# Performance work log

Hardware: AMD Instinct MI355X
Metric: run time of the kernel (lower is better)

The kernel has to match this reference:

```python
import jax, jax.numpy as jnp
import numpy as np

V, E, H, K, B, T = 50000, 128, 256, 9, 128, 512
HD = H // 2  # hidden per direction


def setup_inputs() -> dict:
    key = jax.random.key(0)
    ks = jax.random.split(key, 16)
    s = 0.1
    inp = {
        "x": jax.random.randint(ks[0], (B, T), 0, V),
        "emb": jax.random.normal(ks[1], (V, E), jnp.float32) * 0.02,
        "w_ih_f": jax.random.normal(ks[2], (4 * HD, E), jnp.float32) * s,
        "w_hh_f": jax.random.normal(ks[3], (4 * HD, HD), jnp.float32) * s,
        "b_ih_f": jax.random.normal(ks[4], (4 * HD,), jnp.float32) * s,
        "b_hh_f": jax.random.normal(ks[5], (4 * HD,), jnp.float32) * s,
        "w_ih_b": jax.random.normal(ks[6], (4 * HD, E), jnp.float32) * s,
        "w_hh_b": jax.random.normal(ks[7], (4 * HD, HD), jnp.float32) * s,
        "b_ih_b": jax.random.normal(ks[8], (4 * HD,), jnp.float32) * s,
        "b_hh_b": jax.random.normal(ks[9], (4 * HD,), jnp.float32) * s,
        "W_tag": jax.random.normal(ks[10], (K, H), jnp.float32) * s,
        "b_tag": jax.random.normal(ks[11], (K,), jnp.float32) * s,
        "start_trans": jax.random.normal(ks[12], (K,), jnp.float32) * s,
        "end_trans": jax.random.normal(ks[13], (K,), jnp.float32) * s,
        "trans": jax.random.normal(ks[14], (K, K), jnp.float32) * s,
    }
    return inp


def _lstm_dir(xs, w_ih, w_hh, b_ih, b_hh, reverse):
    # xs: [T, B, E]; PyTorch gate order: i, f, g, o
    Bsz = xs.shape[1]
    hd = w_hh.shape[1]
    b = b_ih + b_hh

    def step(carry, x_t):
        h, c = carry
        gates = x_t @ w_ih.T + h @ w_hh.T + b  # [B, 4*hd]
        i, f, g, o = jnp.split(gates, 4, axis=-1)
        i = jax.nn.sigmoid(i)
        f = jax.nn.sigmoid(f)
        g = jnp.tanh(g)
        o = jax.nn.sigmoid(o)
        c = f * c + i * g
        h = o * jnp.tanh(c)
        return (h, c), h

    init = (jnp.zeros((Bsz, hd), xs.dtype), jnp.zeros((Bsz, hd), xs.dtype))
    _, hs = jax.lax.scan(step, init, xs, reverse=reverse)
    return hs  # [T, B, hd], time-ordered


def _viterbi(emissions, start_trans, end_trans, trans):
    # emissions: [T, B, K]; returns best tag path [B, T] (torchcrf decode, no mask)
    score0 = start_trans[None, :] + emissions[0]  # [B, K]

    def step(score, emis_t):
        # score[b, i] + trans[i, j] -> best over i
        cand = score[:, :, None] + trans[None, :, :]  # [B, K, K]
        bp = jnp.argmax(cand, axis=1)                 # [B, K] best prev tag
        best = jnp.max(cand, axis=1)
        return best + emis_t, bp

    final_score, bps = jax.lax.scan(step, score0, emissions[1:])  # bps: [T-1, B, K]
    final_score = final_score + end_trans[None, :]
    last_tag = jnp.argmax(final_score, axis=-1)  # [B]

    def back(tag, bp):
        prev = jnp.take_along_axis(bp, tag[:, None], axis=1)[:, 0]
        return prev, prev

    _, path = jax.lax.scan(back, last_tag, bps, reverse=True)  # [T-1, B]
    tags = jnp.concatenate([path, last_tag[None, :]], axis=0)  # [T, B]
    return tags.T.astype(jnp.int32)  # [B, T]


def reference(x, emb, w_ih_f, w_hh_f, b_ih_f, b_hh_f,
              w_ih_b, w_hh_b, b_ih_b, b_hh_b,
              W_tag, b_tag, start_trans, end_trans, trans):
    xt = x.T                        # [T, B]
    e = emb[xt]                     # [T, B, E] embedding gather
    h_f = _lstm_dir(e, w_ih_f, w_hh_f, b_ih_f, b_hh_f, reverse=False)
    h_b = _lstm_dir(e, w_ih_b, w_hh_b, b_ih_b, b_hh_b, reverse=True)
    h = jnp.concatenate([h_f, h_b], axis=-1)  # [T, B, H]
    # dropout is identity at inference
    emissions = h @ W_tag.T + b_tag           # [T, B, K]
    return _viterbi(emissions, start_trans, end_trans, trans)
```

## Files before the change

kernel.cpp:

```cpp
#include <hip/hip_runtime.h>
#include <math.h>

#define TT 512
#define BB 128
#define KK 9

__device__ __forceinline__ float fast_sigmoid(float x) {
    const float LOG2E = 1.4426950408889634f;
    float e = __builtin_amdgcn_exp2f(-x * LOG2E);
    return __builtin_amdgcn_rcpf(1.0f + e);
}
__device__ __forceinline__ float fast_tanh(float x) {
    const float LOG2E = 1.4426950408889634f;
    float a = fabsf(x);
    float e = __builtin_amdgcn_exp2f(-2.0f * a * LOG2E);
    float t = (1.0f - e) * __builtin_amdgcn_rcpf(1.0f + e);
    return copysignf(t, x);
}

__global__ __launch_bounds__(256, 3) void input_gemm(
    const int* __restrict__ x, const float* __restrict__ emb,
    const float* __restrict__ w_ih_f, const float* __restrict__ w_ih_b,
    const float* __restrict__ b_ih_f, const float* __restrict__ b_hh_f,
    const float* __restrict__ b_ih_b, const float* __restrict__ b_hh_b,
    float* __restrict__ buf_f, float* __restrict__ buf_b,
    int t0f, int t0b)
{
    const int dir = blockIdx.z;
    const int s   = blockIdx.x;
    const int n0  = blockIdx.y * 128;
    const int t   = (dir ? t0b : t0f) + s;
    const float* w  = dir ? w_ih_b : w_ih_f;
    const float* bi = dir ? b_ih_b : b_ih_f;
    const float* bh = dir ? b_hh_b : b_hh_f;
    float* dst = dir ? buf_b : buf_f;

    __shared__ __align__(16) float As[32][132];
    __shared__ __align__(16) float Bs[32][132];

    const int tid  = threadIdx.x;
    const int lrow = tid >> 3;
    const int k4   = (tid & 7) * 4;

    int tokr[4];
    #pragma unroll
    for (int p = 0; p < 4; p++) tokr[p] = x[(p * 32 + lrow) * TT + t];

    const int tx = tid & 15;
    const int ty = tid >> 4;

    float acc[8][8];
    #pragma unroll
    for (int i = 0; i < 8; i++)
        #pragma unroll
        for (int j = 0; j < 8; j++) acc[i][j] = 0.0f;

    float4 aS[4], bS[4];
    #pragma unroll
    for (int p = 0; p < 4; p++) {
        aS[p] = *(const float4*)(emb + (size_t)tokr[p] * 128 + k4);
        bS[p] = *(const float4*)(w + (size_t)(n0 + p * 32 + lrow) * 128 + k4);
    }

    for (int kc = 0; kc < 128; kc += 32) {
        __syncthreads();
        #pragma unroll
        for (int p = 0; p < 4; p++) {
            const int row = p * 32 + lrow;
            As[k4 + 0][row] = aS[p].x; As[k4 + 1][row] = aS[p].y;
            As[k4 + 2][row] = aS[p].z; As[k4 + 3][row] = aS[p].w;
            Bs[k4 + 0][row] = bS[p].x; Bs[k4 + 1][row] = bS[p].y;
            Bs[k4 + 2][row] = bS[p].z; Bs[k4 + 3][row] = bS[p].w;
        }
        __syncthreads();
        if (kc + 32 < 128) {
            #pragma unroll
            for (int p = 0; p < 4; p++) {
                aS[p] = *(const float4*)(emb + (size_t)tokr[p] * 128 + kc + 32 + k4);
                bS[p] = *(const float4*)(w + (size_t)(n0 + p * 32 + lrow) * 128 + kc + 32 + k4);
            }
        }
        #pragma unroll 8
        for (int k = 0; k < 32; k++) {
            float4 af0 = *(const float4*)&As[k][ty * 8];
            float4 af1 = *(const float4*)&As[k][ty * 8 + 4];
            float4 bf0 = *(const float4*)&Bs[k][tx * 4];
            float4 bf1 = *(const float4*)&Bs[k][64 + tx * 4];
            float a_[8] = {af0.x, af0.y, af0.z, af0.w, af1.x, af1.y, af1.z, af1.w};
            float b_[8] = {bf0.x, bf0.y, bf0.z, bf0.w, bf1.x, bf1.y, bf1.z, bf1.w};
            #pragma unroll
            for (int i = 0; i < 8; i++)
                #pragma unroll
                for (int j = 0; j < 8; j++)
                    acc[i][j] += a_[i] * b_[j];
        }
    }

    const int nb0 = n0 + tx * 4;
    const int nb1 = n0 + 64 + tx * 4;
    float bias[8];
    #pragma unroll
    for (int j = 0; j < 4; j++) {
        bias[j]     = bi[nb0 + j] + bh[nb0 + j];
        bias[4 + j] = bi[nb1 + j] + bh[nb1 + j];
    }
    #pragma unroll
    for (int i = 0; i < 8; i++) {
        int brow = ty * 8 + i;
        float* o = dst + ((size_t)s * 128 + brow) * 512;
        float4 v0, v1;
        v0.x = acc[i][0] + bias[0]; v0.y = acc[i][1] + bias[1];
        v0.z = acc[i][2] + bias[2]; v0.w = acc[i][3] + bias[3];
        v1.x = acc[i][4] + bias[4]; v1.y = acc[i][5] + bias[5];
        v1.z = acc[i][6] + bias[6]; v1.w = acc[i][7] + bias[7];
        *(float4*)(o + nb0) = v0;
        *(float4*)(o + nb1) = v1;
    }
}

__global__ __launch_bounds__(512, 2) void lstm_fused(
    const float* __restrict__ buf_f, const float* __restrict__ buf_b,
    const float* __restrict__ w_hh_f, const float* __restrict__ w_hh_b,
    float* __restrict__ h_all,
    float* __restrict__ h_state, float* __restrict__ c_state,
    const float* __restrict__ W_tag, const float* __restrict__ b_tag,
    const float* __restrict__ start_trans, const float* __restrict__ end_trans,
    const float* __restrict__ trans,
    float* __restrict__ emB, unsigned* __restrict__ flags,
    int* __restrict__ out,
    int t0f, int t0b, int C, int init, int tail)
{
    const int dir = blockIdx.x >> 7;
    const int b   = blockIdx.x & 127;
    const int j   = threadIdx.x;
    const int w_  = j >> 6;
    const int l   = j & 63;
    const int m   = l >> 2;
    const int q   = l & 3;
    const int k   = w_ * 16 + m;
    const int r   = q * 128 + k;

    unsigned snap = 0u;
    if (tail && dir == 0 && j == 0)
        snap = __hip_atomic_load(&flags[b], __ATOMIC_RELAXED, __HIP_MEMORY_SCOPE_AGENT);

    const float* whh = dir ? w_hh_b : w_hh_f;
    float wR[128];
    #pragma unroll
    for (int qq = 0; qq < 32; qq++) {
        float4 v = *(const float4*)(whh + (size_t)r * 128 + qq * 4);
        wR[4*qq+0] = v.x; wR[4*qq+1] = v.y; wR[4*qq+2] = v.z; wR[4*qq+3] = v.w;
    }

    __shared__ __align__(16) float h_lds[2][128];
    __shared__ __align__(16) float wt_s[KK * 132];
    __shared__ __align__(16) float em_s[TT * KK];
    __shared__ __align__(16) float h_tile[64 * 132];
    __shared__ unsigned char bp[TT][KK];

    float c;
    if (init) {
        c = 0.0f;
        if (q == 0) h_lds[0][k] = 0.0f;
    } else {
        c = c_state[((size_t)dir * 128 + b) * 128 + k];
        if (q == 0) h_lds[0][k] = h_state[((size_t)dir * 128 + b) * 128 + k];
    }
    __syncthreads();

    const float* buf = dir ? buf_b : buf_f;
    const int t0     = dir ? t0b : t0f;
    const int  tl0   = dir ? (C - 1) : 0;
    const long lstep = dir ? -(long)(128 * 512) : (long)(128 * 512);

    const float* xp = buf + ((size_t)tl0 * 128 + b) * 512 + r;
    float xw = *xp;
    float h_reg = 0.0f;

    float* hdst = h_all + (size_t)(dir * BB + b) * TT * 128;

    for (int s = 0; s < C; s++) {
        const int t = t0 + (dir ? (C - 1 - s) : s);
        const int p = s & 1;
        const float* hprev = h_lds[p];

        float a0 = 0.f, a1 = 0.f, a2 = 0.f, a3 = 0.f;
        #pragma unroll
        for (int qq = 0; qq < 32; qq++) {
            float4 h4 = *(const float4*)&hprev[4 * qq];
            a0 += wR[4*qq+0] * h4.x;
            a1 += wR[4*qq+1] * h4.y;
            a2 += wR[4*qq+2] * h4.z;
            a3 += wR[4*qq+3] * h4.w;
        }
        float pre = xw + ((a0 + a1) + (a2 + a3));

        float act = (q == 2) ? fast_tanh(pre) : fast_sigmoid(pre);

        float f_ = __shfl_xor(act, 1);
        float g_ = __shfl_xor(act, 2);
        float o_ = __shfl_xor(act, 3);

        c = f_ * c + act * g_;
        h_reg = o_ * fast_tanh(c);
        if (q == 0) h_lds[p ^ 1][k] = h_reg;

        __syncthreads();

        if (s + 1 < C) { xp += lstep; xw = *xp; }
        if (q == 0)
            hdst[(size_t)t * 128 + k] = h_reg;
    }

    if (q == 0) {
        h_state[((size_t)dir * 128 + b) * 128 + k] = h_reg;
        c_state[((size_t)dir * 128 + b) * 128 + k] = c;
    }

    if (!tail) return;

    for (int f = j; f < KK * 128; f += 512)
        wt_s[(f >> 7) * 132 + (f & 127)] = W_tag[(f >> 7) * 256 + dir * 128 + (f & 127)];

    float* emdst = emB + (size_t)b * TT * KK;

    for (int tile = 0; tile < TT / 64; tile++) {
        const int tb = tile * 64;
        __syncthreads();
        #pragma unroll
        for (int it = 0; it < 4; it++) {
            const int f4 = it * 512 + j;
            const int tr = f4 >> 5;
            const int c4 = (f4 & 31) * 4;
            float4 v = *(const float4*)(hdst + (size_t)(tb + tr) * 128 + c4);
            *(float4*)&h_tile[tr * 132 + c4] = v;
        }
        __syncthreads();
        for (int task = j; task < 64 * KK; task += 512) {
            const int tl = task / 9;
            const int kk = task - tl * 9;
            const float* hp = &h_tile[tl * 132];
            const float* wp = &wt_s[kk * 132];
            float acc = 0.0f;
            #pragma unroll
            for (int i4 = 0; i4 < 32; i4++) {
                float4 h4 = *(const float4*)(hp + i4 * 4);
                float4 w4 = *(const float4*)(wp + i4 * 4);
                acc += h4.x * w4.x + h4.y * w4.y + h4.z * w4.z + h4.w * w4.w;
            }
            if (dir == 1) emdst[(size_t)tb * KK + task] = acc;
            else          em_s[tb * KK + task] = acc;
        }
    }
    __syncthreads();

    if (dir == 1) {
        if (j == 0) {
            __threadfence();
            __hip_atomic_fetch_add(&flags[b], 1u, __ATOMIC_RELEASE,
                                   __HIP_MEMORY_SCOPE_AGENT);
        }
        return;
    }

    if (j == 0) {
        while (__hip_atomic_load(&flags[b], __ATOMIC_ACQUIRE,
                                 __HIP_MEMORY_SCOPE_AGENT) == snap)
            __builtin_amdgcn_s_sleep(1);
    }
    __syncthreads();
    for (int f = j; f < TT * KK; f += 512)
        em_s[f] += emdst[f] + b_tag[f % KK];
    __syncthreads();

    if (j < 64) {
        const int lane = j;

        float trans_col[KK];
        float score = -1e30f;
        if (lane < KK) {
            #pragma unroll
            for (int i = 0; i < KK; i++) trans_col[i] = trans[i * KK + lane];
            score = start_trans[lane] + em_s[lane];
        }

        float em_cur = (lane < KK) ? em_s[KK + lane] : 0.0f;
        for (int t = 1; t < TT; t++) {
            float em_next = (t + 1 < TT && lane < KK) ? em_s[(t + 1) * KK + lane] : 0.0f;

            float my = (lane < KK) ? score : -1e30f;
            float cand[KK];
            #pragma unroll
            for (int i = 0; i < KK; i++) cand[i] = __shfl(my, i) + trans_col[i];

            float v01, v23, v45, v67, v03, v47, v07, vb_;
            int   i01, i23, i45, i67, i03, i47, i07, ib_;
            {
                bool gt;
                gt = cand[1] > cand[0]; v01 = gt ? cand[1] : cand[0]; i01 = gt ? 1 : 0;
                gt = cand[3] > cand[2]; v23 = gt ? cand[3] : cand[2]; i23 = gt ? 3 : 2;
                gt = cand[5] > cand[4]; v45 = gt ? cand[5] : cand[4]; i45 = gt ? 5 : 4;
                gt = cand[7] > cand[6]; v67 = gt ? cand[7] : cand[6]; i67 = gt ? 7 : 6;
                gt = v23 > v01; v03 = gt ? v23 : v01; i03 = gt ? i23 : i01;
                gt = v67 > v45; v47 = gt ? v67 : v45; i47 = gt ? i67 : i45;
                gt = v47 > v03; v07 = gt ? v47 : v03; i07 = gt ? i47 : i03;
                gt = cand[8] > v07; vb_ = gt ? cand[8] : v07; ib_ = gt ? 8 : i07;
            }

            if (lane < KK) {
                bp[t][lane] = (unsigned char)ib_;
                score = vb_ + em_cur;
            }
            em_cur = em_next;
        }

        float fin = (lane < KK) ? (score + end_trans[lane]) : -1e30f;
        float farr[KK];
        #pragma unroll
        for (int jx = 0; jx < KK; jx++) farr[jx] = __shfl(fin, jx);
        float v01, v23, v45, v67, v03, v47, v07, vb_;
        int   i01, i23, i45, i67, i03, i47, i07, bj;
        {
            bool gt;
            gt = farr[1] > farr[0]; v01 = gt ? farr[1] : farr[0]; i01 = gt ? 1 : 0;
            gt = farr[3] > farr[2]; v23 = gt ? farr[3] : farr[2]; i23 = gt ? 3 : 2;
            gt = farr[5] > farr[4]; v45 = gt ? farr[5] : farr[4]; i45 = gt ? 5 : 4;
            gt = farr[7] > farr[6]; v67 = gt ? farr[7] : farr[6]; i67 = gt ? 7 : 6;
            gt = v23 > v01; v03 = gt ? v23 : v01; i03 = gt ? i23 : i01;
            gt = v67 > v45; v47 = gt ? v67 : v45; i47 = gt ? i67 : i45;
            gt = v47 > v03; v07 = gt ? v47 : v03; i07 = gt ? i47 : i03;
            gt = farr[8] > v07; vb_ = gt ? farr[8] : v07; bj = gt ? 8 : i07;
        }

        if (lane == 0) {
            int tag = bj;
            out[b * TT + (TT - 1)] = tag;
            for (int t = TT - 1; t >= 1; t--) {
                tag = bp[t][tag];
                out[b * TT + t - 1] = tag;
            }
        }
    }
}

extern "C" void kernel_launch(void* const* d_in, const int* in_sizes, int n_in,
                              void* d_out, int out_size, void* d_ws, size_t ws_size,
                              hipStream_t stream)
{
    const int*   x       = (const int*)  d_in[0];
    const float* emb     = (const float*)d_in[1];
    const float* w_ih_f  = (const float*)d_in[2];
    const float* w_hh_f  = (const float*)d_in[3];
    const float* b_ih_f  = (const float*)d_in[4];
    const float* b_hh_f  = (const float*)d_in[5];
    const float* w_ih_b  = (const float*)d_in[6];
    const float* w_hh_b  = (const float*)d_in[7];
    const float* b_ih_b  = (const float*)d_in[8];
    const float* b_hh_b  = (const float*)d_in[9];
    const float* W_tag   = (const float*)d_in[10];
    const float* b_tag   = (const float*)d_in[11];
    const float* start_t = (const float*)d_in[12];
    const float* end_t   = (const float*)d_in[13];
    const float* trans   = (const float*)d_in[14];
    int* out = (int*)d_out;

    const size_t em_elems    = (size_t)BB * TT * KK;
    const size_t state_elems = (size_t)2 * 128 * 128;
    const size_t hall_elems  = (size_t)2 * BB * TT * 128;

    int C = 32;
    const int cands[5] = {512, 256, 128, 64, 32};
    for (int ci = 0; ci < 5; ci++) {
        size_t need = ((size_t)2 * cands[ci] * BB * 512
                       + em_elems + 2 * state_elems + hall_elems) * sizeof(float)
                      + 1024;
        if (ws_size >= need) { C = cands[ci]; break; }
    }

    float* buf_f   = (float*)d_ws;
    float* buf_b   = buf_f + (size_t)C * BB * 512;
    float* emB     = buf_b + (size_t)C * BB * 512;
    float* h_state = emB + em_elems;
    float* c_state = h_state + state_elems;
    float* h_all   = c_state + state_elems;
    unsigned* flags = (unsigned*)(h_all + hall_elems);

    const int rounds = TT / C;
    for (int r = 0; r < rounds; r++) {
        const int t0f = r * C;
        const int t0b = TT - (r + 1) * C;
        dim3 gg(C, 4, 2);
        input_gemm<<<gg, dim3(256), 0, stream>>>(
            x, emb, w_ih_f, w_ih_b, b_ih_f, b_hh_f, b_ih_b, b_hh_b,
            buf_f, buf_b, t0f, t0b);
        lstm_fused<<<dim3(256), dim3(512), 0, stream>>>(
            buf_f, buf_b, w_hh_f, w_hh_b, h_all,
            h_state, c_state,
            W_tag, b_tag, start_t, end_t, trans,
            emB, flags, out,
            t0f, t0b, C, (r == 0) ? 1 : 0, (r == rounds - 1) ? 1 : 0);
    }
}
```

Measured before the change: 847.2 us.

## Compute two timesteps per input-GEMM block to reuse the weight tile

Measured after the change: 854.3 us. About the same (+0.8%).

```diff
diff --git a/kernel.cpp b/kernel.cpp
--- a/kernel.cpp
+++ b/kernel.cpp
@@ -18,7 +18,7 @@
     return copysignf(t, x);
 }
 
-__global__ __launch_bounds__(256, 3) void input_gemm(
+__global__ __launch_bounds__(256, 2) void input_gemm(
     const int* __restrict__ x, const float* __restrict__ emb,
     const float* __restrict__ w_ih_f, const float* __restrict__ w_ih_b,
     const float* __restrict__ b_ih_f, const float* __restrict__ b_hh_f,
@@ -27,39 +27,45 @@
     int t0f, int t0b)
 {
     const int dir = blockIdx.z;
-    const int s   = blockIdx.x;
+    const int s0  = blockIdx.x * 2;
     const int n0  = blockIdx.y * 128;
-    const int t   = (dir ? t0b : t0f) + s;
+    const int tA  = (dir ? t0b : t0f) + s0;
+    const int tB  = tA + 1;
     const float* w  = dir ? w_ih_b : w_ih_f;
     const float* bi = dir ? b_ih_b : b_ih_f;
     const float* bh = dir ? b_hh_b : b_hh_f;
     float* dst = dir ? buf_b : buf_f;
 
-    __shared__ __align__(16) float As[32][132];
-    __shared__ __align__(16) float Bs[32][132];
+    __shared__ __align__(16) float A0s[32 * 133];
+    __shared__ __align__(16) float A1s[32 * 133];
+    __shared__ __align__(16) float Bs [32 * 133];
 
     const int tid  = threadIdx.x;
     const int lrow = tid >> 3;
     const int k4   = (tid & 7) * 4;
 
-    int tokr[4];
-    #pragma unroll
-    for (int p = 0; p < 4; p++) tokr[p] = x[(p * 32 + lrow) * TT + t];
+    int tok0[4], tok1[4];
+    #pragma unroll
+    for (int p = 0; p < 4; p++) {
+        tok0[p] = x[(p * 32 + lrow) * TT + tA];
+        tok1[p] = x[(p * 32 + lrow) * TT + tB];
+    }
 
     const int tx = tid & 15;
     const int ty = tid >> 4;
 
-    float acc[8][8];
+    float acc0[8][8], acc1[8][8];
     #pragma unroll
     for (int i = 0; i < 8; i++)
         #pragma unroll
-        for (int j = 0; j < 8; j++) acc[i][j] = 0.0f;
-
-    float4 aS[4], bS[4];
+        for (int j = 0; j < 8; j++) { acc0[i][j] = 0.0f; acc1[i][j] = 0.0f; }
+
+    float4 a0S[4], a1S[4], bS[4];
     #pragma unroll
     for (int p = 0; p < 4; p++) {
-        aS[p] = *(const float4*)(emb + (size_t)tokr[p] * 128 + k4);
-        bS[p] = *(const float4*)(w + (size_t)(n0 + p * 32 + lrow) * 128 + k4);
+        a0S[p] = *(const float4*)(emb + (size_t)tok0[p] * 128 + k4);
+        a1S[p] = *(const float4*)(emb + (size_t)tok1[p] * 128 + k4);
+        bS[p]  = *(const float4*)(w + (size_t)(n0 + p * 32 + lrow) * 128 + k4);
     }
 
     for (int kc = 0; kc < 128; kc += 32) {
@@ -67,32 +73,46 @@
         #pragma unroll
         for (int p = 0; p < 4; p++) {
             const int row = p * 32 + lrow;
-            As[k4 + 0][row] = aS[p].x; As[k4 + 1][row] = aS[p].y;
-            As[k4 + 2][row] = aS[p].z; As[k4 + 3][row] = aS[p].w;
-            Bs[k4 + 0][row] = bS[p].x; Bs[k4 + 1][row] = bS[p].y;
-            Bs[k4 + 2][row] = bS[p].z; Bs[k4 + 3][row] = bS[p].w;
+            A0s[(k4 + 0) * 133 + row] = a0S[p].x;
+            A0s[(k4 + 1) * 133 + row] = a0S[p].y;
+            A0s[(k4 + 2) * 133 + row] = a0S[p].z;
+            A0s[(k4 + 3) * 133 + row] = a0S[p].w;
+            A1s[(k4 + 0) * 133 + row] = a1S[p].x;
+            A1s[(k4 + 1) * 133 + row] = a1S[p].y;
+            A1s[(k4 + 2) * 133 + row] = a1S[p].z;
+            A1s[(k4 + 3) * 133 + row] = a1S[p].w;
+            Bs [(k4 + 0) * 133 + row] = bS[p].x;
+            Bs [(k4 + 1) * 133 + row] = bS[p].y;
+            Bs [(k4 + 2) * 133 + row] = bS[p].z;
+            Bs [(k4 + 3) * 133 + row] = bS[p].w;
         }
         __syncthreads();
         if (kc + 32 < 128) {
             #pragma unroll
             for (int p = 0; p < 4; p++) {
-                aS[p] = *(const float4*)(emb + (size_t)tokr[p] * 128 + kc + 32 + k4);
-                bS[p] = *(const float4*)(w + (size_t)(n0 + p * 32 + lrow) * 128 + kc + 32 + k4);
+                a0S[p] = *(const float4*)(emb + (size_t)tok0[p] * 128 + kc + 32 + k4);
+                a1S[p] = *(const float4*)(emb + (size_t)tok1[p] * 128 + kc + 32 + k4);
+                bS[p]  = *(const float4*)(w + (size_t)(n0 + p * 32 + lrow) * 128 + kc + 32 + k4);
             }
         }
-        #pragma unroll 8
+        #pragma unroll 4
         for (int k = 0; k < 32; k++) {
-            float4 af0 = *(const float4*)&As[k][ty * 8];
-            float4 af1 = *(const float4*)&As[k][ty * 8 + 4];
-            float4 bf0 = *(const float4*)&Bs[k][tx * 4];
-            float4 bf1 = *(const float4*)&Bs[k][64 + tx * 4];
-            float a_[8] = {af0.x, af0.y, af0.z, af0.w, af1.x, af1.y, af1.z, af1.w};
+            float4 bf0 = *(const float4*)&Bs[k * 133 + tx * 4];
+            float4 bf1 = *(const float4*)&Bs[k * 133 + 64 + tx * 4];
+            float4 a00 = *(const float4*)&A0s[k * 133 + ty * 8];
+            float4 a01 = *(const float4*)&A0s[k * 133 + ty * 8 + 4];
+            float4 a10 = *(const float4*)&A1s[k * 133 + ty * 8];
+            float4 a11 = *(const float4*)&A1s[k * 133 + ty * 8 + 4];
             float b_[8] = {bf0.x, bf0.y, bf0.z, bf0.w, bf1.x, bf1.y, bf1.z, bf1.w};
+            float p0[8] = {a00.x, a00.y, a00.z, a00.w, a01.x, a01.y, a01.z, a01.w};
+            float p1[8] = {a10.x, a10.y, a10.z, a10.w, a11.x, a11.y, a11.z, a11.w};
             #pragma unroll
             for (int i = 0; i < 8; i++)
                 #pragma unroll
-                for (int j = 0; j < 8; j++)
-                    acc[i][j] += a_[i] * b_[j];
+                for (int j = 0; j < 8; j++) {
+                    acc0[i][j] += p0[i] * b_[j];
+                    acc1[i][j] += p1[i] * b_[j];
+                }
         }
     }
 
@@ -107,14 +127,21 @@
     #pragma unroll
     for (int i = 0; i < 8; i++) {
         int brow = ty * 8 + i;
-        float* o = dst + ((size_t)s * 128 + brow) * 512;
-        float4 v0, v1;
-        v0.x = acc[i][0] + bias[0]; v0.y = acc[i][1] + bias[1];
-        v0.z = acc[i][2] + bias[2]; v0.w = acc[i][3] + bias[3];
-        v1.x = acc[i][4] + bias[4]; v1.y = acc[i][5] + bias[5];
-        v1.z = acc[i][6] + bias[6]; v1.w = acc[i][7] + bias[7];
-        *(float4*)(o + nb0) = v0;
-        *(float4*)(o + nb1) = v1;
+        float* o0 = dst + ((size_t)s0 * 128 + brow) * 512;
+        float* o1 = o0 + (size_t)128 * 512;
+        float4 v;
+        v.x = acc0[i][0] + bias[0]; v.y = acc0[i][1] + bias[1];
+        v.z = acc0[i][2] + bias[2]; v.w = acc0[i][3] + bias[3];
+        *(float4*)(o0 + nb0) = v;
+        v.x = acc0[i][4] + bias[4]; v.y = acc0[i][5] + bias[5];
+        v.z = acc0[i][6] + bias[6]; v.w = acc0[i][7] + bias[7];
+        *(float4*)(o0 + nb1) = v;
+        v.x = acc1[i][0] + bias[0]; v.y = acc1[i][1] + bias[1];
+        v.z = acc1[i][2] + bias[2]; v.w = acc1[i][3] + bias[3];
+        *(float4*)(o1 + nb0) = v;
+        v.x = acc1[i][4] + bias[4]; v.y = acc1[i][5] + bias[5];
+        v.z = acc1[i][6] + bias[6]; v.w = acc1[i][7] + bias[7];
+        *(float4*)(o1 + nb1) = v;
     }
 }
 
@@ -389,7 +416,7 @@
     for (int r = 0; r < rounds; r++) {
         const int t0f = r * C;
         const int t0b = TT - (r + 1) * C;
-        dim3 gg(C, 4, 2);
+        dim3 gg(C / 2, 4, 2);
         input_gemm<<<gg, dim3(256), 0, stream>>>(
             x, emb, w_ih_f, w_ih_b, b_ih_f, b_hh_f, b_ih_b, b_hh_b,
             buf_f, buf_b, t0f, t0b);
```

## Parallelize Viterbi backtrace with pointer-jumping scan over backpointer maps

Applied to the files above, without the earlier changes.

Measured after the change: 877.5 us. 1.04x slower.

```diff
diff --git a/kernel.cpp b/kernel.cpp
--- a/kernel.cpp
+++ b/kernel.cpp
@@ -157,6 +157,7 @@
     __shared__ __align__(16) float em_s[TT * KK];
     __shared__ __align__(16) float h_tile[64 * 132];
     __shared__ unsigned char bp[TT][KK];
+    __shared__ int bj_s;
 
     float c;
     if (init) {
@@ -333,13 +334,36 @@
         }
 
         if (lane == 0) {
-            int tag = bj;
-            out[b * TT + (TT - 1)] = tag;
-            for (int t = TT - 1; t >= 1; t--) {
-                tag = bp[t][tag];
-                out[b * TT + t - 1] = tag;
+            bj_s = bj;
+            out[b * TT + (TT - 1)] = bj;
+        }
+    }
+    __syncthreads();
+
+    {
+        unsigned char* mA = (unsigned char*)h_tile;
+        unsigned char* mB = mA + TT * KK;
+        #pragma unroll
+        for (int i = 0; i < KK; i++)
+            mA[j * KK + i] = (j >= 1) ? bp[j][i] : (unsigned char)0;
+        __syncthreads();
+        for (int kk = 1; kk < TT; kk <<= 1) {
+            if (j >= 1) {
+                if (j + kk < TT) {
+                    #pragma unroll
+                    for (int i = 0; i < KK; i++)
+                        mB[j * KK + i] = mA[j * KK + mA[(j + kk) * KK + i]];
+                } else {
+                    #pragma unroll
+                    for (int i = 0; i < KK; i++)
+                        mB[j * KK + i] = mA[j * KK + i];
+                }
             }
-        }
+            __syncthreads();
+            unsigned char* tmp = mA; mA = mB; mB = tmp;
+        }
+        if (j >= 1)
+            out[b * TT + (j - 1)] = mA[j * KK + bj_s];
     }
 }
 
```
